# Optimization experiments

Measured on AMD Instinct MI355X. Metric: run time of the kernel, lower is better.

Reference implementation:

```python
import jax, jax.numpy as jnp
import numpy as np

B, T, D, H = 4, 1024, 1024, 16
NUM_BUCKETS = 320
MAX_DIST = 800
LN_EPS = 1e-5


def _rel_bucket(T):
    # bidirectional T5-style relative position buckets
    ctx = jnp.arange(T)[:, None]
    mem = jnp.arange(T)[None, :]
    rel = mem - ctx  # (T, T)
    half = NUM_BUCKETS // 2  # 160
    bucket = (rel > 0).astype(jnp.int32) * half
    n = jnp.abs(rel)
    max_exact = half // 2  # 80
    is_small = n < max_exact
    n_f = jnp.maximum(n, 1).astype(jnp.float32)
    large = max_exact + (
        jnp.log(n_f / max_exact) / np.log(MAX_DIST / max_exact) * (half - max_exact)
    ).astype(jnp.int32)
    large = jnp.minimum(large, half - 1)
    return bucket + jnp.where(is_small, n, large)


def setup_inputs() -> dict:
    key = jax.random.key(0)
    ks = jax.random.split(key, 12)
    s = 0.02
    return {
        "x": jax.random.normal(ks[0], (B, T, D), jnp.float32),
        "ln_w": jnp.ones((D,), jnp.float32),
        "ln_b": jnp.zeros((D,), jnp.float32),
        "wq": jax.random.normal(ks[1], (D, D), jnp.float32) * s,
        "bq": jnp.zeros((D,), jnp.float32),
        "wk": jax.random.normal(ks[2], (D, D), jnp.float32) * s,
        "bk": jnp.zeros((D,), jnp.float32),
        "wv": jax.random.normal(ks[3], (D, D), jnp.float32) * s,
        "bv": jnp.zeros((D,), jnp.float32),
        "wo": jax.random.normal(ks[4], (D, D), jnp.float32) * s,
        "bo": jnp.zeros((D,), jnp.float32),
        "rel_emb": jax.random.normal(ks[5], (NUM_BUCKETS, H), jnp.float32) * s,
        "grep_w": jax.random.normal(ks[6], (8, D // H), jnp.float32) * s,
        "grep_b": jnp.zeros((8,), jnp.float32),
        "grep_a": jnp.ones((1, H, 1, 1), jnp.float32),
    }


def reference(x, ln_w, ln_b, wq, bq, wk, bk, wv, bv, wo, bo, rel_emb, grep_w, grep_b, grep_a):
    Bb, Tt, Dd = x.shape
    hd = Dd // H
    scaling = hd ** -0.5
    # pre-norm LayerNorm
    mu = jnp.mean(x, -1, keepdims=True)
    var = jnp.mean((x - mu) ** 2, -1, keepdims=True)
    h = (x - mu) / jnp.sqrt(var + LN_EPS) * ln_w + ln_b
    # projections (q pre-scaled as in fairseq/WavLM)
    q = (h @ wq.T + bq) * scaling
    k = h @ wk.T + bk
    v = h @ wv.T + bv
    q = q.reshape(Bb, Tt, H, hd).transpose(0, 2, 1, 3)  # (B,H,T,hd)
    k = k.reshape(Bb, Tt, H, hd).transpose(0, 2, 1, 3)
    v = v.reshape(Bb, Tt, H, hd).transpose(0, 2, 1, 3)
    # bucketed relative position bias: (H, T, T)
    buckets = _rel_bucket(Tt)
    pos_bias = rel_emb[buckets].transpose(2, 0, 1)
    # gru_rel_pos gating (per batch, head, query position)
    alpha = 32.0
    ql = q * (alpha / scaling)  # undo scaling, multiply by alpha
    g = jax.nn.sigmoid((ql @ grep_w.T + grep_b).reshape(Bb, H, Tt, 2, 4).sum(-1))
    gate_a, gate_b = g[..., 0:1], g[..., 1:2]  # (B,H,T,1)
    gate = gate_a * (gate_b * grep_a - 1.0) + 2.0
    # attention
    scores = jnp.einsum('bhtd,bhsd->bhts', q, k) + gate * pos_bias[None]
    attn = jax.nn.softmax(scores, axis=-1)
    out = jnp.einsum('bhts,bhsd->bhtd', attn, v).transpose(0, 2, 1, 3).reshape(Bb, Tt, Dd)
    # output projection, dropout (identity in eval), residual
    out = out @ wo.T + bo + x
    pos_bias_out = jnp.broadcast_to(pos_bias[None], (Bb, H, Tt, Tt)).reshape(Bb * H, Tt, Tt)
    return out, pos_bias_out
```

## Files before the change

kernel.cpp:

```cpp
#include <hip/hip_runtime.h>

typedef unsigned short u16;
typedef __attribute__((ext_vector_type(8))) short short8;
typedef __attribute__((ext_vector_type(4))) short short4v;
typedef __attribute__((ext_vector_type(4))) float floatx4;

#define MFMA16(a, b, c) __builtin_amdgcn_mfma_f32_16x16x32_bf16(a, b, c, 0, 0, 0)

__device__ __forceinline__ float bf2f(u16 u) {
  return __uint_as_float(((unsigned int)u) << 16);
}
__device__ __forceinline__ u16 f2bf(float f) {
  unsigned int u = __float_as_uint(f);
  unsigned int r = (u + 0x7fffu + ((u >> 16) & 1u)) >> 16;
  return (u16)r;
}
__device__ __forceinline__ void gl_lds16(const u16* g, u16* lds_wave_base) {
  __builtin_amdgcn_global_load_lds(
      (const __attribute__((address_space(1))) unsigned int*)g,
      (__attribute__((address_space(3))) unsigned int*)lds_wave_base, 16, 0, 0);
}

__global__ __launch_bounds__(256) void ln_kernel(
    const float* __restrict__ x, const float* __restrict__ w, const float* __restrict__ bb,
    u16* __restrict__ hb)
{
  int wid = threadIdx.x >> 6, lane = threadIdx.x & 63;
  int row = blockIdx.x * 4 + wid;
  const float* xr = x + row * 1024 + lane * 16;
  float xs[16];
#pragma unroll
  for (int i = 0; i < 4; i++) {
    float4 v = *(const float4*)(xr + i * 4);
    xs[i * 4 + 0] = v.x; xs[i * 4 + 1] = v.y; xs[i * 4 + 2] = v.z; xs[i * 4 + 3] = v.w;
  }
  float s = 0.f, ss = 0.f;
#pragma unroll
  for (int i = 0; i < 16; i++) { s += xs[i]; ss += xs[i] * xs[i]; }
#pragma unroll
  for (int m = 1; m < 64; m <<= 1) { s += __shfl_xor(s, m, 64); ss += __shfl_xor(ss, m, 64); }
  float mu = s * (1.0f / 1024.0f);
  float var = ss * (1.0f / 1024.0f) - mu * mu;
  float rstd = rsqrtf(var + 1e-5f);
  const float* wr = w + lane * 16;
  const float* br = bb + lane * 16;
  short8 o0, o1;
#pragma unroll
  for (int i = 0; i < 8; i++) {
    o0[i] = (short)f2bf((xs[i] - mu) * rstd * wr[i] + br[i]);
    o1[i] = (short)f2bf((xs[8 + i] - mu) * rstd * wr[8 + i] + br[8 + i]);
  }
  u16* hr = hb + row * 1024 + lane * 16;
  *(short8*)hr = o0;
  *(short8*)(hr + 8) = o1;
}

__global__ __launch_bounds__(256) void convw_kernel(
    const float* __restrict__ wq, const float* __restrict__ wk,
    const float* __restrict__ wv, const float* __restrict__ wo,
    u16* __restrict__ wb)
{
  int idx = (blockIdx.x * 256 + threadIdx.x) * 8;
  int seg = idx >> 20, off = idx & 1048575;
  const float* s = (seg == 0) ? wq : (seg == 1) ? wk : (seg == 2) ? wv : wo;
  float4 f0 = *(const float4*)(s + off);
  float4 f1 = *(const float4*)(s + off + 4);
  short8 o;
  o[0] = (short)f2bf(f0.x); o[1] = (short)f2bf(f0.y);
  o[2] = (short)f2bf(f0.z); o[3] = (short)f2bf(f0.w);
  o[4] = (short)f2bf(f1.x); o[5] = (short)f2bf(f1.y);
  o[6] = (short)f2bf(f1.z); o[7] = (short)f2bf(f1.w);
  *(short8*)&wb[idx] = o;
}

__global__ __launch_bounds__(256) void qkv_kernel(
    const u16* __restrict__ hb, const u16* __restrict__ wb,
    const float* __restrict__ bq, const float* __restrict__ bk, const float* __restrict__ bv,
    u16* __restrict__ qs, u16* __restrict__ kko, u16* __restrict__ vraw)
{
  __shared__ u16 As[128 * 32];
  __shared__ u16 Bs[128 * 32];
  int tid = threadIdx.x;
  int wid = tid >> 6, lane = tid & 63;
  int wm = wid >> 1, wn = wid & 1;
  int l15 = lane & 15, quad = lane >> 4;
  int m0 = blockIdx.y * 128;
  int n0g = blockIdx.x * 128;
  int sec = n0g >> 10;
  int n0 = n0g & 1023;
  const u16* W = wb + sec * 1048576;
  const float* bias = (sec == 0) ? bq : ((sec == 1) ? bk : bv);

  floatx4 zero4 = {0.f, 0.f, 0.f, 0.f};
  floatx4 acc[4][4];
#pragma unroll
  for (int i = 0; i < 4; i++)
#pragma unroll
    for (int j = 0; j < 4; j++) acc[i][j] = zero4;

  int lr = tid >> 2;
  int lc = (tid & 3) * 8;
  u16* asw = As + wid * 512;
  u16* bsw = Bs + wid * 512;

  for (int kt = 0; kt < 1024; kt += 32) {
    gl_lds16(&hb[(m0 + lr) * 1024 + kt + lc],      asw);
    gl_lds16(&hb[(m0 + lr + 64) * 1024 + kt + lc], asw + 2048);
    gl_lds16(&W[(n0 + lr) * 1024 + kt + lc],       bsw);
    gl_lds16(&W[(n0 + lr + 64) * 1024 + kt + lc],  bsw + 2048);
    __syncthreads();
    short8 af[4], bf[4];
#pragma unroll
    for (int mi = 0; mi < 4; mi++)
      af[mi] = *(const short8*)&As[(wm * 64 + mi * 16 + l15) * 32 + quad * 8];
#pragma unroll
    for (int ni = 0; ni < 4; ni++)
      bf[ni] = *(const short8*)&Bs[(wn * 64 + ni * 16 + l15) * 32 + quad * 8];
#pragma unroll
    for (int mi = 0; mi < 4; mi++)
#pragma unroll
      for (int ni = 0; ni < 4; ni++)
        acc[mi][ni] = MFMA16(af[mi], bf[ni], acc[mi][ni]);
    __syncthreads();
  }

  int bidx = m0 >> 10;
#pragma unroll
  for (int mi = 0; mi < 4; mi++) {
#pragma unroll
    for (int ni = 0; ni < 4; ni++) {
#pragma unroll
      for (int r = 0; r < 4; r++) {
        int row = m0 + wm * 64 + mi * 16 + quad * 4 + r;
        int t = row & 1023;
        int c = n0 + wn * 64 + ni * 16 + l15;
        float val = acc[mi][ni][r] + bias[c];
        int hh = c >> 6, hp = c & 63;
        int addr = ((bidx * 16 + hh) * 1024 + t) * 64 + hp;
        if (sec == 0) {
          qs[addr] = f2bf(val * 0.125f);
        } else if (sec == 1) {
          kko[addr] = f2bf(val);
        } else {
          vraw[addr] = f2bf(val);
        }
      }
    }
  }
}

__global__ __launch_bounds__(256) void vtrans_kernel(
    const u16* __restrict__ vraw, u16* __restrict__ vt)
{
  __shared__ u16 T[64][72];
  int bh = blockIdx.y;
  int t0 = blockIdx.x * 64;
  const u16* src = vraw + bh * 65536;
  u16* dst = vt + bh * 65536;
  int tid = threadIdx.x;
  int r = tid >> 3;
  int c8 = (tid & 7) * 8;
  short8 a = *(const short8*)&src[(t0 + r) * 64 + c8];
  short8 b = *(const short8*)&src[(t0 + r + 32) * 64 + c8];
  *(short8*)&T[r][c8] = a;
  *(short8*)&T[r + 32][c8] = b;
  __syncthreads();
  int hd = tid >> 3;
  int tl = (tid & 7) * 8;
  short8 o0, o1;
#pragma unroll
  for (int j = 0; j < 8; j++) { o0[j] = (short)T[tl + j][hd]; o1[j] = (short)T[tl + j][hd + 32]; }
  *(short8*)&dst[hd * 1024 + t0 + tl] = o0;
  *(short8*)&dst[(hd + 32) * 1024 + t0 + tl] = o1;
}

__device__ __forceinline__ int rel_bucket(int t, int s) {
  int rel = s - t;
  int bucket = (rel > 0) ? 160 : 0;
  int n = (rel < 0) ? -rel : rel;
  if (n < 80) return bucket + n;
  float a = logf((float)n / 80.0f);
  float c = a / (float)2.302585092994046;
  float v = c * 80.0f;
  int large = 80 + (int)v;
  if (large > 159) large = 159;
  return bucket + large;
}

__global__ __launch_bounds__(256) void bias0_kernel(
    const float* __restrict__ rel_emb, float* __restrict__ out1,
    u16* __restrict__ bh16, int nb4)
{
  int tid = blockIdx.x * 256 + threadIdx.x;
  int t = tid >> 7;
  int s0 = (tid & 127) * 8;
  int bkt[8];
#pragma unroll
  for (int j = 0; j < 8; j++) bkt[j] = rel_bucket(t, s0 + j) * 16;
  int base_ts = t * 1024 + s0;
#pragma unroll
  for (int hh = 0; hh < 16; hh++) {
    float4 v0, v1;
    v0.x = rel_emb[bkt[0] + hh]; v0.y = rel_emb[bkt[1] + hh];
    v0.z = rel_emb[bkt[2] + hh]; v0.w = rel_emb[bkt[3] + hh];
    v1.x = rel_emb[bkt[4] + hh]; v1.y = rel_emb[bkt[5] + hh];
    v1.z = rel_emb[bkt[6] + hh]; v1.w = rel_emb[bkt[7] + hh];
    float* p = out1 + hh * 1048576 + base_ts;
    *(float4*)p = v0;
    *(float4*)(p + 4) = v1;
    if (nb4) {
      *(float4*)(p + 16777216) = v0; *(float4*)(p + 16777216 + 4) = v1;
      *(float4*)(p + 33554432) = v0; *(float4*)(p + 33554432 + 4) = v1;
      *(float4*)(p + 50331648) = v0; *(float4*)(p + 50331648 + 4) = v1;
    }
    short8 o;
    o[0] = (short)f2bf(v0.x); o[1] = (short)f2bf(v0.y);
    o[2] = (short)f2bf(v0.z); o[3] = (short)f2bf(v0.w);
    o[4] = (short)f2bf(v1.x); o[5] = (short)f2bf(v1.y);
    o[6] = (short)f2bf(v1.z); o[7] = (short)f2bf(v1.w);
    *(short8*)(bh16 + hh * 1048576 + base_ts) = o;
  }
}

__global__ __launch_bounds__(256) void bias_copy_kernel(float* __restrict__ out1)
{
  int idx = blockIdx.x * 256 + threadIdx.x;
  float4 v = *(const float4*)&out1[idx * 4];
  *(float4*)&out1[16777216 + idx * 4] = v;
  *(float4*)&out1[33554432 + idx * 4] = v;
  *(float4*)&out1[50331648 + idx * 4] = v;
}

__global__ __launch_bounds__(256, 4) void attn_kernel(
    const u16* __restrict__ qs, const u16* __restrict__ kko, const u16* __restrict__ vt,
    const float* __restrict__ gw, const float* __restrict__ gb, const float* __restrict__ ga,
    const u16* __restrict__ bh16, u16* __restrict__ ao)
{
  __shared__ __align__(16) u16 Pb[4][16 * 72];
  int wid = threadIdx.x >> 6, lane = threadIdx.x & 63;
  int l15 = lane & 15, quad = lane >> 4;
  int bh = blockIdx.y;
  int b = bh >> 4, h = bh & 15;
  int q0 = blockIdx.x * 64 + wid * 16;
  const u16* Q = qs + bh * 65536;
  const u16* K = kko + bh * 65536;
  const u16* V = vt + bh * 65536;
  const u16* Bi = bh16 + h * 1048576;
  u16* pb = &Pb[wid][0];

  const u16* qrow = Q + (q0 + l15) * 64;
  short8 q8[8];
#pragma unroll
  for (int i = 0; i < 8; i++) q8[i] = *(const short8*)&qrow[i * 8];
  float e[8];
#pragma unroll
  for (int i = 0; i < 8; i++) e[i] = gb[i];
#pragma unroll
  for (int i8 = 0; i8 < 8; i8++)
#pragma unroll
    for (int j = 0; j < 8; j++) {
      float ql = bf2f((u16)q8[i8][j]) * 256.0f;
#pragma unroll
      for (int i = 0; i < 8; i++) e[i] += ql * gw[i * 64 + i8 * 8 + j];
    }
  float u0 = e[0] + e[1] + e[2] + e[3];
  float u1 = e[4] + e[5] + e[6] + e[7];
  float sa = 1.0f / (1.0f + __expf(-u0));
  float sb = 1.0f / (1.0f + __expf(-u1));
  float gt = sa * (sb * ga[h] - 1.0f) + 2.0f;

  short8 qf0 = *(const short8*)&Q[(q0 + l15) * 64 + quad * 8];
  short8 qf1 = *(const short8*)&Q[(q0 + l15) * 64 + quad * 8 + 32];
  float mrun = -1e30f, lsum = 0.f;
  floatx4 zero4 = {0.f, 0.f, 0.f, 0.f};
  floatx4 accO[4];
#pragma unroll
  for (int ni = 0; ni < 4; ni++) accO[ni] = zero4;

  for (int s0 = 0; s0 < 1024; s0 += 64) {
    short4v bi4[4];
#pragma unroll
    for (int tile = 0; tile < 4; tile++)
      bi4[tile] = *(const short4v*)&Bi[(q0 + l15) * 1024 + s0 + tile * 16 + quad * 4];
    floatx4 sc[4];
#pragma unroll
    for (int tile = 0; tile < 4; tile++) {
      short8 kf = *(const short8*)&K[(s0 + tile * 16 + l15) * 64 + quad * 8];
      sc[tile] = MFMA16(kf, qf0, zero4);
      kf = *(const short8*)&K[(s0 + tile * 16 + l15) * 64 + quad * 8 + 32];
      sc[tile] = MFMA16(kf, qf1, sc[tile]);
    }
    float v[16];
    float mt = -1e30f;
#pragma unroll
    for (int tile = 0; tile < 4; tile++)
#pragma unroll
      for (int r = 0; r < 4; r++) {
        float val = sc[tile][r] + gt * bf2f((u16)bi4[tile][r]);
        v[tile * 4 + r] = val;
        mt = fmaxf(mt, val);
      }
    mt = fmaxf(mt, __shfl_xor(mt, 16, 64));
    mt = fmaxf(mt, __shfl_xor(mt, 32, 64));
    float mnew = fmaxf(mrun, mt);
    float alpha = __expf(fmaxf(mrun - mnew, -80.0f));
    mrun = mnew;
    float psum = 0.f;
#pragma unroll
    for (int i = 0; i < 16; i++) { v[i] = __expf(v[i] - mnew); psum += v[i]; }
    lsum = lsum * alpha + psum;
#pragma unroll
    for (int ni = 0; ni < 4; ni++) accO[ni] *= alpha;
#pragma unroll
    for (int tile = 0; tile < 4; tile++) {
      short4v o;
#pragma unroll
      for (int r = 0; r < 4; r++) o[r] = (short)f2bf(v[tile * 4 + r]);
      *(short4v*)&pb[l15 * 72 + tile * 16 + quad * 4] = o;
    }
    short8 pf0 = *(const short8*)&pb[l15 * 72 + quad * 8];
    short8 pf1 = *(const short8*)&pb[l15 * 72 + 32 + quad * 8];
#pragma unroll
    for (int ni = 0; ni < 4; ni++) {
      short8 vf = *(const short8*)&V[(ni * 16 + l15) * 1024 + s0 + quad * 8];
      accO[ni] = MFMA16(vf, pf0, accO[ni]);
      vf = *(const short8*)&V[(ni * 16 + l15) * 1024 + s0 + 32 + quad * 8];
      accO[ni] = MFMA16(vf, pf1, accO[ni]);
    }
  }
  lsum += __shfl_xor(lsum, 16, 64);
  lsum += __shfl_xor(lsum, 32, 64);
  float linv = 1.0f / lsum;
#pragma unroll
  for (int ni = 0; ni < 4; ni++) {
    short4v o;
#pragma unroll
    for (int r = 0; r < 4; r++) o[r] = (short)f2bf(accO[ni][r] * linv);
    *(short4v*)&pb[l15 * 72 + ni * 16 + quad * 4] = o;
  }
#pragma unroll
  for (int r = 0; r < 4; r++) {
    int t = q0 + quad * 4 + r;
#pragma unroll
    for (int ni = 0; ni < 4; ni++) {
      u16 val = pb[(quad * 4 + r) * 72 + ni * 16 + l15];
      ao[(b * 1024 + t) * 1024 + h * 64 + ni * 16 + l15] = val;
    }
  }
}

__global__ __launch_bounds__(256) void oproj_kernel(
    const u16* __restrict__ ao, const u16* __restrict__ wob, const float* __restrict__ bo,
    const float* __restrict__ x, float* __restrict__ out)
{
  __shared__ u16 As[128 * 32];
  __shared__ u16 Bs[128 * 32];
  int tid = threadIdx.x;
  int wid = tid >> 6, lane = tid & 63;
  int wm = wid >> 1, wn = wid & 1;
  int l15 = lane & 15, quad = lane >> 4;
  int m0 = blockIdx.y * 128;
  int n0 = blockIdx.x * 128;

  floatx4 zero4 = {0.f, 0.f, 0.f, 0.f};
  floatx4 acc[4][4];
#pragma unroll
  for (int i = 0; i < 4; i++)
#pragma unroll
    for (int j = 0; j < 4; j++) acc[i][j] = zero4;

  int lr = tid >> 2;
  int lc = (tid & 3) * 8;
  u16* asw = As + wid * 512;
  u16* bsw = Bs + wid * 512;

  for (int kt = 0; kt < 1024; kt += 32) {
    gl_lds16(&ao[(m0 + lr) * 1024 + kt + lc],       asw);
    gl_lds16(&ao[(m0 + lr + 64) * 1024 + kt + lc],  asw + 2048);
    gl_lds16(&wob[(n0 + lr) * 1024 + kt + lc],      bsw);
    gl_lds16(&wob[(n0 + lr + 64) * 1024 + kt + lc], bsw + 2048);
    __syncthreads();
    short8 af[4], bf[4];
#pragma unroll
    for (int mi = 0; mi < 4; mi++)
      af[mi] = *(const short8*)&As[(wm * 64 + mi * 16 + l15) * 32 + quad * 8];
#pragma unroll
    for (int ni = 0; ni < 4; ni++)
      bf[ni] = *(const short8*)&Bs[(wn * 64 + ni * 16 + l15) * 32 + quad * 8];
#pragma unroll
    for (int mi = 0; mi < 4; mi++)
#pragma unroll
      for (int ni = 0; ni < 4; ni++)
        acc[mi][ni] = MFMA16(af[mi], bf[ni], acc[mi][ni]);
    __syncthreads();
  }

#pragma unroll
  for (int mi = 0; mi < 4; mi++) {
#pragma unroll
    for (int ni = 0; ni < 4; ni++) {
#pragma unroll
      for (int r = 0; r < 4; r++) {
        int row = m0 + wm * 64 + mi * 16 + quad * 4 + r;
        int c = n0 + wn * 64 + ni * 16 + l15;
        out[row * 1024 + c] = acc[mi][ni][r] + bo[c] + x[row * 1024 + c];
      }
    }
  }
}

extern "C" void kernel_launch(void* const* d_in, const int* in_sizes, int n_in,
                              void* d_out, int out_size, void* d_ws, size_t ws_size,
                              hipStream_t stream) {
  const float* x    = (const float*)d_in[0];
  const float* ln_w = (const float*)d_in[1];
  const float* ln_b = (const float*)d_in[2];
  const float* wq   = (const float*)d_in[3];
  const float* bq   = (const float*)d_in[4];
  const float* wk   = (const float*)d_in[5];
  const float* bk   = (const float*)d_in[6];
  const float* wv   = (const float*)d_in[7];
  const float* bv   = (const float*)d_in[8];
  const float* wo   = (const float*)d_in[9];
  const float* bo   = (const float*)d_in[10];
  const float* rel  = (const float*)d_in[11];
  const float* gw   = (const float*)d_in[12];
  const float* gb   = (const float*)d_in[13];
  const float* ga   = (const float*)d_in[14];

  float* out0  = (float*)d_out;
  float* out1f = out0 + 4194304;

  int big_ws = (ws_size >= (size_t)(128u << 20)) ? 1 : 0;
  char* sb = big_ws ? (char*)d_ws : (char*)(out1f + 16777216);
  u16* hbb  = (u16*)(sb);
  u16* wbb  = (u16*)(sb + (8u << 20));
  u16* qsb  = (u16*)(sb + (16u << 20));
  u16* kkb  = (u16*)(sb + (24u << 20));
  u16* vtb  = (u16*)(sb + (32u << 20));
  u16* aob  = (u16*)(sb + (40u << 20));
  u16* bhb  = (u16*)(sb + (48u << 20));
  u16* vrw  = (u16*)(sb + (80u << 20));

  ln_kernel<<<1024, 256, 0, stream>>>(x, ln_w, ln_b, hbb);
  convw_kernel<<<2048, 256, 0, stream>>>(wq, wk, wv, wo, wbb);
  qkv_kernel<<<dim3(24, 32), 256, 0, stream>>>(hbb, wbb, bq, bk, bv, qsb, kkb, vrw);
  vtrans_kernel<<<dim3(16, 64), 256, 0, stream>>>(vrw, vtb);
  bias0_kernel<<<512, 256, 0, stream>>>(rel, out1f, bhb, big_ws);
  attn_kernel<<<dim3(16, 64), 256, 0, stream>>>(qsb, kkb, vtb, gw, gb, ga, bhb, aob);
  oproj_kernel<<<dim3(8, 32), 256, 0, stream>>>(aob, wbb + 3145728, bo, x, out0);
  if (!big_ws)
    bias_copy_kernel<<<16384, 256, 0, stream>>>(out1f);
}
```

Baseline: 568.8 us.

## Split attention over key chunks with separate gate and combine kernels

The attention kernel now handles a quarter of the key range per block, across a third grid dimension, instead of looping over all 1024 keys. It writes unnormalized fp32 partial outputs plus per-row max and sum to a workspace. A new combine kernel merges the four partials with log-sum-exp weights and writes the bf16 attention output. The gating sigmoid also moves out of attention into a standalone gate kernel. The intent is more blocks in flight and shorter serial loops, at the cost of a large fp32 partial buffer to write and read back, two extra launches, and a bigger workspace threshold.

Measured after the change: 587.5 us. 1.03x slower.

```diff
diff --git a/kernel.cpp b/kernel.cpp
--- a/kernel.cpp
+++ b/kernel.cpp
@@ -231,16 +231,44 @@
   *(float4*)&out1[50331648 + idx * 4] = v;
 }
 
+__global__ __launch_bounds__(256) void gate_kernel(
+    const u16* __restrict__ qs, const float* __restrict__ gw, const float* __restrict__ gb,
+    const float* __restrict__ ga, float* __restrict__ gate)
+{
+  int idx = blockIdx.x * 256 + threadIdx.x;
+  int h = (idx >> 10) & 15;
+  const u16* qv = qs + idx * 64;
+  float e[8];
+#pragma unroll
+  for (int i = 0; i < 8; i++) e[i] = gb[i];
+#pragma unroll
+  for (int i8 = 0; i8 < 8; i8++) {
+    short8 q8 = *(const short8*)&qv[i8 * 8];
+#pragma unroll
+    for (int j = 0; j < 8; j++) {
+      float ql = bf2f((u16)q8[j]) * 256.0f;
+#pragma unroll
+      for (int i = 0; i < 8; i++) e[i] += ql * gw[i * 64 + i8 * 8 + j];
+    }
+  }
+  float u0 = e[0] + e[1] + e[2] + e[3];
+  float u1 = e[4] + e[5] + e[6] + e[7];
+  float sa = 1.0f / (1.0f + __expf(-u0));
+  float sb = 1.0f / (1.0f + __expf(-u1));
+  gate[idx] = sa * (sb * ga[h] - 1.0f) + 2.0f;
+}
+
 __global__ __launch_bounds__(256, 4) void attn_kernel(
     const u16* __restrict__ qs, const u16* __restrict__ kko, const u16* __restrict__ vt,
-    const float* __restrict__ gw, const float* __restrict__ gb, const float* __restrict__ ga,
-    const u16* __restrict__ bh16, u16* __restrict__ ao)
+    const float* __restrict__ gate, const u16* __restrict__ bh16,
+    float* __restrict__ op, float* __restrict__ mp, float* __restrict__ lp)
 {
   __shared__ __align__(16) u16 Pb[4][16 * 72];
   int wid = threadIdx.x >> 6, lane = threadIdx.x & 63;
   int l15 = lane & 15, quad = lane >> 4;
   int bh = blockIdx.y;
-  int b = bh >> 4, h = bh & 15;
+  int h = bh & 15;
+  int sp = blockIdx.z;
   int q0 = blockIdx.x * 64 + wid * 16;
   const u16* Q = qs + bh * 65536;
   const u16* K = kko + bh * 65536;
@@ -248,26 +276,7 @@
   const u16* Bi = bh16 + h * 1048576;
   u16* pb = &Pb[wid][0];
 
-  const u16* qrow = Q + (q0 + l15) * 64;
-  short8 q8[8];
-#pragma unroll
-  for (int i = 0; i < 8; i++) q8[i] = *(const short8*)&qrow[i * 8];
-  float e[8];
-#pragma unroll
-  for (int i = 0; i < 8; i++) e[i] = gb[i];
-#pragma unroll
-  for (int i8 = 0; i8 < 8; i8++)
-#pragma unroll
-    for (int j = 0; j < 8; j++) {
-      float ql = bf2f((u16)q8[i8][j]) * 256.0f;
-#pragma unroll
-      for (int i = 0; i < 8; i++) e[i] += ql * gw[i * 64 + i8 * 8 + j];
-    }
-  float u0 = e[0] + e[1] + e[2] + e[3];
-  float u1 = e[4] + e[5] + e[6] + e[7];
-  float sa = 1.0f / (1.0f + __expf(-u0));
-  float sb = 1.0f / (1.0f + __expf(-u1));
-  float gt = sa * (sb * ga[h] - 1.0f) + 2.0f;
+  float gt = gate[bh * 1024 + q0 + l15];
 
   short8 qf0 = *(const short8*)&Q[(q0 + l15) * 64 + quad * 8];
   short8 qf1 = *(const short8*)&Q[(q0 + l15) * 64 + quad * 8 + 32];
@@ -277,7 +286,10 @@
 #pragma unroll
   for (int ni = 0; ni < 4; ni++) accO[ni] = zero4;
 
-  for (int s0 = 0; s0 < 1024; s0 += 64) {
+  int sbeg = sp * 256;
+#pragma unroll
+  for (int it = 0; it < 4; it++) {
+    int s0 = sbeg + it * 64;
     short4v bi4[4];
 #pragma unroll
     for (int tile = 0; tile < 4; tile++)
@@ -330,23 +342,63 @@
   }
   lsum += __shfl_xor(lsum, 16, 64);
   lsum += __shfl_xor(lsum, 32, 64);
-  float linv = 1.0f / lsum;
-#pragma unroll
-  for (int ni = 0; ni < 4; ni++) {
-    short4v o;
-#pragma unroll
-    for (int r = 0; r < 4; r++) o[r] = (short)f2bf(accO[ni][r] * linv);
-    *(short4v*)&pb[l15 * 72 + ni * 16 + quad * 4] = o;
-  }
-#pragma unroll
-  for (int r = 0; r < 4; r++) {
-    int t = q0 + quad * 4 + r;
-#pragma unroll
-    for (int ni = 0; ni < 4; ni++) {
-      u16 val = pb[(quad * 4 + r) * 72 + ni * 16 + l15];
-      ao[(b * 1024 + t) * 1024 + h * 64 + ni * 16 + l15] = val;
-    }
-  }
+  float* opb = op + ((sp * 64 + bh) * 64) * 1024;
+#pragma unroll
+  for (int ni = 0; ni < 4; ni++)
+#pragma unroll
+    for (int r = 0; r < 4; r++)
+      opb[(ni * 16 + quad * 4 + r) * 1024 + q0 + l15] = accO[ni][r];
+  if (quad == 0) {
+    mp[(sp * 64 + bh) * 1024 + q0 + l15] = mrun;
+    lp[(sp * 64 + bh) * 1024 + q0 + l15] = lsum;
+  }
+}
+
+__global__ __launch_bounds__(256) void combine_kernel(
+    const float* __restrict__ op, const float* __restrict__ mp, const float* __restrict__ lp,
+    u16* __restrict__ ao)
+{
+  __shared__ u16 T[64][68];
+  int t0 = blockIdx.x * 64;
+  int bh = blockIdx.y;
+  int b = bh >> 4, h = bh & 15;
+  int tid = threadIdx.x;
+  int lt = tid & 63;
+  int wid = tid >> 6;
+  int t = t0 + lt;
+  float m[4], l[4];
+#pragma unroll
+  for (int i = 0; i < 4; i++) {
+    m[i] = mp[(i * 64 + bh) * 1024 + t];
+    l[i] = lp[(i * 64 + bh) * 1024 + t];
+  }
+  float M = fmaxf(fmaxf(m[0], m[1]), fmaxf(m[2], m[3]));
+  float w[4], L = 0.f;
+#pragma unroll
+  for (int i = 0; i < 4; i++) { w[i] = __expf(m[i] - M); L += l[i] * w[i]; }
+  float inv = 1.0f / L;
+#pragma unroll
+  for (int k = 0; k < 16; k++) {
+    int hd = wid * 16 + k;
+    float o = 0.f;
+#pragma unroll
+    for (int i = 0; i < 4; i++)
+      o += op[((i * 64 + bh) * 64 + hd) * 1024 + t] * w[i];
+    T[lt][hd] = f2bf(o * inv);
+  }
+  __syncthreads();
+  int tr = tid >> 2;
+  int c16 = (tid & 3) * 16;
+  short4v a0 = *(const short4v*)&T[tr][c16];
+  short4v a1 = *(const short4v*)&T[tr][c16 + 4];
+  short4v a2 = *(const short4v*)&T[tr][c16 + 8];
+  short4v a3 = *(const short4v*)&T[tr][c16 + 12];
+  short8 o0, o1;
+#pragma unroll
+  for (int i = 0; i < 4; i++) { o0[i] = a0[i]; o0[4 + i] = a1[i]; o1[i] = a2[i]; o1[4 + i] = a3[i]; }
+  u16* dst = &ao[(b * 1024 + t0 + tr) * 1024 + h * 64 + c16];
+  *(short8*)dst = o0;
+  *(short8*)(dst + 8) = o1;
 }
 
 __global__ __launch_bounds__(256) void oproj_kernel(
@@ -431,23 +483,29 @@
   float* out0  = (float*)d_out;
   float* out1f = out0 + 4194304;
 
-  int big_ws = (ws_size >= (size_t)(128u << 20)) ? 1 : 0;
+  int big_ws = (ws_size >= (size_t)(192u << 20)) ? 1 : 0;
   char* sb = big_ws ? (char*)d_ws : (char*)(out1f + 16777216);
-  u16* hbb  = (u16*)(sb);
-  u16* wbb  = (u16*)(sb + (8u << 20));
-  u16* qsb  = (u16*)(sb + (16u << 20));
-  u16* kkb  = (u16*)(sb + (24u << 20));
-  u16* vtb  = (u16*)(sb + (32u << 20));
-  u16* aob  = (u16*)(sb + (40u << 20));
-  u16* bhb  = (u16*)(sb + (48u << 20));
-  u16* vrw  = (u16*)(sb + (80u << 20));
+  u16* hbb   = (u16*)(sb);
+  u16* wbb   = (u16*)(sb + (8u << 20));
+  u16* qsb   = (u16*)(sb + (16u << 20));
+  u16* kkb   = (u16*)(sb + (24u << 20));
+  u16* vtb   = (u16*)(sb + (32u << 20));
+  u16* aob   = (u16*)(sb + (40u << 20));
+  u16* bhb   = (u16*)(sb + (48u << 20));
+  u16* vrw   = (u16*)(sb + (80u << 20));
+  float* opb = (float*)(sb + (88u << 20));
+  float* mpb = (float*)(sb + (152u << 20));
+  float* lpb = (float*)(sb + (153u << 20));
+  float* gtb = (float*)(sb + (154u << 20));
 
   ln_kernel<<<1024, 256, 0, stream>>>(x, ln_w, ln_b, hbb);
   convw_kernel<<<2048, 256, 0, stream>>>(wq, wk, wv, wo, wbb);
   qkv_kernel<<<dim3(24, 32), 256, 0, stream>>>(hbb, wbb, bq, bk, bv, qsb, kkb, vrw);
   vtrans_kernel<<<dim3(16, 64), 256, 0, stream>>>(vrw, vtb);
   bias0_kernel<<<512, 256, 0, stream>>>(rel, out1f, bhb, big_ws);
-  attn_kernel<<<dim3(16, 64), 256, 0, stream>>>(qsb, kkb, vtb, gw, gb, ga, bhb, aob);
+  gate_kernel<<<256, 256, 0, stream>>>(qsb, gw, gb, ga, gtb);
+  attn_kernel<<<dim3(16, 64, 4), 256, 0, stream>>>(qsb, kkb, vtb, gtb, bhb, opb, mpb, lpb);
+  combine_kernel<<<dim3(16, 64), 256, 0, stream>>>(opb, mpb, lpb, aob);
   oproj_kernel<<<dim3(8, 32), 256, 0, stream>>>(aob, wbb + 3145728, bo, x, out0);
   if (!big_ws)
     bias_copy_kernel<<<16384, 256, 0, stream>>>(out1f);
```
